# Optimization experiments

Hardware: AMD Instinct MI355X
Metric: run time of the kernel (lower is better)

The kernel has to match this reference:

```python
import jax, jax.numpy as jnp
import numpy as np

B, L, D = 2, 2048, 1024
H, DH = 16, 64
SCALE = 1.0 / np.sqrt(DH).astype(np.float32)
NEG = -1e9


def setup_inputs() -> dict:
    key = jax.random.key(0)
    ks = jax.random.split(key, 12)
    s = 0.02
    x = jax.random.normal(ks[0], (B, L, D), jnp.float32)
    lattice = jax.random.normal(ks[1], (B, 6), jnp.float32)
    B_graph = jax.random.normal(ks[2], (B, L, L), jnp.float32) * 0.05
    # causal additive mask [L, L]
    attn_mask = jnp.where(jnp.tril(jnp.ones((L, L), bool)), 0.0, NEG).astype(jnp.float32)
    Wq = jax.random.normal(ks[3], (D, H * DH), jnp.float32) * s
    bq = jnp.zeros((H * DH,), jnp.float32)
    Wk = jax.random.normal(ks[4], (D, H * DH), jnp.float32) * s
    bk = jnp.zeros((H * DH,), jnp.float32)
    Wv = jax.random.normal(ks[5], (D, H * DH), jnp.float32) * s
    bv = jnp.zeros((H * DH,), jnp.float32)
    Wo = jax.random.normal(ks[6], (H * DH, D), jnp.float32) * s
    bo = jnp.zeros((D,), jnp.float32)
    Wl = jax.random.normal(ks[7], (6, H), jnp.float32) * s
    bl = jnp.zeros((H,), jnp.float32)
    return {"x": x, "lattice": lattice, "B_graph": B_graph, "attn_mask": attn_mask,
            "Wq": Wq, "bq": bq, "Wk": Wk, "bk": bk, "Wv": Wv, "bv": bv,
            "Wo": Wo, "bo": bo, "Wl": Wl, "bl": bl}


def reference(x, lattice, B_graph, attn_mask, Wq, bq, Wk, bk, Wv, bv, Wo, bo, Wl, bl):
    b, l, d = x.shape
    # projections -> [b, h, l, dh]
    q = (x @ Wq + bq).reshape(b, l, H, DH).transpose(0, 2, 1, 3)
    k = (x @ Wk + bk).reshape(b, l, H, DH).transpose(0, 2, 1, 3)
    v = (x @ Wv + bv).reshape(b, l, H, DH).transpose(0, 2, 1, 3)
    scores = jnp.einsum('bhid,bhjd->bhij', q, k) * SCALE
    lattice_bias = lattice @ Wl + bl          # [b, h]
    scores = scores + lattice_bias[:, :, None, None]
    scores = scores + B_graph[:, None, :, :]   # [b,1,l,l]
    scores = scores + attn_mask[None, None, :, :]
    attn = jax.nn.softmax(scores.astype(jnp.float32), axis=-1).astype(scores.dtype)
    out = jnp.einsum('bhij,bhjd->bhid', attn, v)
    out = out.transpose(0, 2, 1, 3).reshape(b, l, H * DH)
    out = out @ Wo + bo
    return (out, attn)
```

## Files before the change

### kernel.cpp

```cpp
#include <hip/hip_runtime.h>
#include <stdint.h>
#include <stddef.h>

#define BB 2
#define LL 2048
#define DD 1024
#define HH 16
#define DHH 64
#define NH 1024

typedef __attribute__((ext_vector_type(8))) __bf16 bf16x8;
typedef __attribute__((ext_vector_type(4))) float f32x4;

__device__ __forceinline__ f32x4 mfma_bf16(bf16x8 a, bf16x8 b, f32x4 c) {
    return __builtin_amdgcn_mfma_f32_16x16x32_bf16(a, b, c, 0, 0, 0);
}

__device__ __forceinline__ unsigned short f2bf(float f) {
    union { float f; unsigned u; } v; v.f = f;
    unsigned r = v.u + 0x7FFFu + ((v.u >> 16) & 1u);
    return (unsigned short)(r >> 16);
}

__device__ __forceinline__ float bf2f(unsigned short s) {
    union { unsigned u; float f; } v; v.u = ((unsigned)s) << 16;
    return v.f;
}

__device__ __forceinline__ bf16x8 ld_frag(const unsigned short* p) {
    return *reinterpret_cast<const bf16x8*>(p);
}

__global__ __launch_bounds__(256)
void conv_x_kernel(const float* __restrict__ x, unsigned short* __restrict__ xb)
{
    const size_t i = ((size_t)blockIdx.x * 256 + threadIdx.x) * 8;
    float4 a = *(const float4*)(x + i);
    float4 b = *(const float4*)(x + i + 4);
    unsigned short t[8];
    t[0] = f2bf(a.x); t[1] = f2bf(a.y); t[2] = f2bf(a.z); t[3] = f2bf(a.w);
    t[4] = f2bf(b.x); t[5] = f2bf(b.y); t[6] = f2bf(b.z); t[7] = f2bf(b.w);
    *(int4*)(xb + i) = *(const int4*)t;
}

__global__ __launch_bounds__(256)
void conv_w_kernel(const float* __restrict__ W0, const float* __restrict__ W1,
                   const float* __restrict__ W2, const float* __restrict__ W3,
                   unsigned short* __restrict__ Wqkvt,
                   unsigned short* __restrict__ Wot)
{
    __shared__ unsigned short Ls[64][72];
    const int which = blockIdx.z;
    const float* W = (which == 0) ? W0 : (which == 1) ? W1 : (which == 2) ? W2 : W3;
    unsigned short* Wt = (which == 3) ? Wot : (Wqkvt + (size_t)which * 1024 * 1024);

    const int kt = blockIdx.x * 64, nt = blockIdx.y * 64;
    const int tid = threadIdx.x;

    {
        const int r = tid >> 2, c = (tid & 3) * 16;
        const float* wp = W + (size_t)(kt + r) * 1024 + nt + c;
        unsigned short t[16];
#pragma unroll
        for (int q = 0; q < 4; ++q) {
            float4 f = *(const float4*)(wp + q * 4);
            t[q * 4 + 0] = f2bf(f.x); t[q * 4 + 1] = f2bf(f.y);
            t[q * 4 + 2] = f2bf(f.z); t[q * 4 + 3] = f2bf(f.w);
        }
        *(int4*)&Ls[r][c]     = *(const int4*)&t[0];
        *(int4*)&Ls[r][c + 8] = *(const int4*)&t[8];
    }
    __syncthreads();
    {
        const int nr = tid >> 2, kc = (tid & 3) * 16;
        unsigned short t[16];
#pragma unroll
        for (int m = 0; m < 16; ++m) t[m] = Ls[kc + m][nr];
        unsigned short* op = Wt + (size_t)(nt + nr) * 1024 + kt + kc;
        *(int4*)op       = *(const int4*)&t[0];
        *(int4*)(op + 8) = *(const int4*)&t[8];
    }
}

template<int MODE>
__global__ __launch_bounds__(256)
void gemm128_kernel(const unsigned short* __restrict__ A,
                    const unsigned short* __restrict__ Bt,
                    const float* __restrict__ b0, const float* __restrict__ b1,
                    const float* __restrict__ b2,
                    void* __restrict__ outp)
{
    __shared__ __align__(16) unsigned short As[128][64];
    __shared__ __align__(16) unsigned short Bs[128][64];

    const int tid  = threadIdx.x;
    const int lane = tid & 63;
    const int w    = tid >> 6;
    const int wr   = w >> 1, wc = w & 1;
    const int l16  = lane & 15, lk = lane >> 4;

    const int m0 = blockIdx.y * 128;
    const int n0 = blockIdx.x * 128;

    const int r8  = tid >> 3;
    const int cb  = tid & 7;
    const int swz = cb ^ (r8 & 7);

    const unsigned short* Ap = A  + (size_t)m0 * 1024 + cb * 8;
    const unsigned short* Bp = Bt + (size_t)n0 * 1024 + cb * 8;

    f32x4 acc[4][4];
#pragma unroll
    for (int i = 0; i < 4; ++i)
#pragma unroll
        for (int j = 0; j < 4; ++j) acc[i][j] = f32x4{0.f, 0.f, 0.f, 0.f};

    for (int k0 = 0; k0 < 1024; k0 += 64) {
        __syncthreads();
#pragma unroll
        for (int c = 0; c < 4; ++c) {
            const int row = c * 32 + r8;
            bf16x8 av = ld_frag(Ap + (size_t)row * 1024 + k0);
            bf16x8 bv = ld_frag(Bp + (size_t)row * 1024 + k0);
            *(bf16x8*)&As[row][swz * 8] = av;
            *(bf16x8*)&Bs[row][swz * 8] = bv;
        }
        __syncthreads();

#pragma unroll
        for (int kk = 0; kk < 2; ++kk) {
            bf16x8 af[4], bfr[4];
#pragma unroll
            for (int fm = 0; fm < 4; ++fm) {
                const int row = wr * 64 + fm * 16 + l16;
                const int kb  = kk * 4 + lk;
                af[fm] = ld_frag(&As[row][(kb ^ (row & 7)) * 8]);
            }
#pragma unroll
            for (int fn = 0; fn < 4; ++fn) {
                const int row = wc * 64 + fn * 16 + l16;
                const int kb  = kk * 4 + lk;
                bfr[fn] = ld_frag(&Bs[row][(kb ^ (row & 7)) * 8]);
            }
#pragma unroll
            for (int fm = 0; fm < 4; ++fm)
#pragma unroll
                for (int fn = 0; fn < 4; ++fn)
                    acc[fm][fn] = mfma_bf16(af[fm], bfr[fn], acc[fm][fn]);
        }
    }

    if (MODE == 0) {
        const int which = n0 >> 10;
        const float* bias = (which == 0) ? b0 : (which == 1) ? b1 : b2;
        unsigned short* out = (unsigned short*)outp
                            + (size_t)which * ((size_t)BB * HH * LL * DHH);
        const int c00 = n0 & 1023;
#pragma unroll
        for (int fm = 0; fm < 4; ++fm)
#pragma unroll
            for (int fn = 0; fn < 4; ++fn)
#pragma unroll
                for (int r = 0; r < 4; ++r) {
                    const int grow = m0 + wr * 64 + fm * 16 + lk * 4 + r;
                    const int c    = c00 + wc * 64 + fn * 16 + l16;
                    const float v  = acc[fm][fn][r] + bias[c];
                    const int b = grow >> 11, i = grow & 2047;
                    const int h = c >> 6,     d = c & 63;
                    out[(((size_t)(b * HH + h)) * LL + i) * DHH + d] = f2bf(v);
                }
    } else {
        float* out = (float*)outp;
#pragma unroll
        for (int fm = 0; fm < 4; ++fm)
#pragma unroll
            for (int fn = 0; fn < 4; ++fn)
#pragma unroll
                for (int r = 0; r < 4; ++r) {
                    const int grow = m0 + wr * 64 + fm * 16 + lk * 4 + r;
                    const int gcol = n0 + wc * 64 + fn * 16 + l16;
                    out[(size_t)grow * DD + gcol] = acc[fm][fn][r] + b0[gcol];
                }
    }
}

__global__ __launch_bounds__(256)
void v_transpose_kernel(const unsigned short* __restrict__ vws,
                        unsigned short* __restrict__ vT)
{
    __shared__ unsigned short Ls[64][72];
    const int bh = blockIdx.y;
    const int i0 = blockIdx.x * 64;
    const int tid = threadIdx.x;

    {
        const int r = tid >> 2, c = (tid & 3) * 16;
        const unsigned short* vp = vws + ((size_t)bh * LL + i0 + r) * DHH + c;
        *(int4*)&Ls[r][c]     = *(const int4*)vp;
        *(int4*)&Ls[r][c + 8] = *(const int4*)(vp + 8);
    }
    __syncthreads();
    {
        const int d = tid >> 2, c = (tid & 3) * 16;
        unsigned short tmp[16];
#pragma unroll
        for (int m = 0; m < 16; ++m) tmp[m] = Ls[c + m][d];
        unsigned short* op = vT + ((size_t)bh * DHH + d) * LL + i0 + c;
        *(int4*)op       = *(const int4*)&tmp[0];
        *(int4*)(op + 8) = *(const int4*)&tmp[8];
    }
}

__global__ __launch_bounds__(128, 4)
void attn_kernel(const unsigned short* __restrict__ qws,
                 const unsigned short* __restrict__ kws,
                 const unsigned short* __restrict__ vT,
                 const float* __restrict__ B_graph,
                 const float* __restrict__ lattice,
                 const float* __restrict__ Wl,
                 const float* __restrict__ bl,
                 float* __restrict__ attn_out,
                 unsigned short* __restrict__ out_pre)
{
    const int n  = blockIdx.x;
    const int bh = n & 31;
    const int tb = n >> 5;
    const int kg = tb >> 3, tt = tb & 7;
    const int ib = 8 * kg + ((kg & 1) ? 7 - tt : tt);
    const int b = bh >> 4, h = bh & 15;
    const int i0 = ib * 32;
    const int nj = (ib >> 1) + 1;

    __shared__ unsigned short Ps[2][16][72];

    const int tid  = threadIdx.x;
    const int lane = tid & 63;
    const int w    = tid >> 6;
    const int l16  = lane & 15, lk = lane >> 4;

    float lb = bl[h];
#pragma unroll
    for (int t = 0; t < 6; ++t) lb += lattice[b * 6 + t] * Wl[t * HH + h];

    const int bhh = b * HH + h;
    const unsigned short* qbase = qws + ((size_t)bhh * LL + i0) * DHH;
    const unsigned short* kbase = kws + (size_t)bhh * LL * DHH;
    const unsigned short* vtb   = vT + (size_t)bhh * DHH * LL;
    const float* gb = B_graph + (size_t)b * LL * LL;

    bf16x8 qa0 = ld_frag(qbase + (size_t)(w * 16 + l16) * DHH + lk * 8);
    bf16x8 qa1 = ld_frag(qbase + (size_t)(w * 16 + l16) * DHH + 32 + lk * 8);

    const int gi0 = i0 + w * 16 + lk * 4;

    float s_run[4];
#pragma unroll
    for (int r = 0; r < 4; ++r) s_run[r] = 0.f;

    auto loadK = [&](int jb, bf16x8* kb) {
        const unsigned short* kt = kbase + (size_t)jb * 64 * DHH;
#pragma unroll
        for (int fn = 0; fn < 4; ++fn) {
            kb[2 * fn]     = ld_frag(kt + (size_t)(fn * 16 + l16) * DHH + lk * 8);
            kb[2 * fn + 1] = ld_frag(kt + (size_t)(fn * 16 + l16) * DHH + 32 + lk * 8);
        }
    };

    auto accumTile = [&](int jb, const bf16x8* kb) {
#pragma unroll
        for (int fn = 0; fn < 4; ++fn) {
            f32x4 z = {0.f, 0.f, 0.f, 0.f};
            z = mfma_bf16(qa0, kb[2 * fn], z);
            z = mfma_bf16(qa1, kb[2 * fn + 1], z);
            const int gj = jb * 64 + fn * 16 + l16;
#pragma unroll
            for (int r = 0; r < 4; ++r) {
                const int gi = gi0 + r;
                const float sv = fmaf(z[r], 0.125f, lb + gb[(size_t)gi * LL + gj]);
                s_run[r] += (gj > gi) ? 0.f : __expf(sv);
            }
        }
    };

    {
        int jb = 0;
        for (; jb + 2 <= nj; jb += 2) {
            bf16x8 k0[8], k1[8];
            loadK(jb, k0);
            loadK(jb + 1, k1);
            accumTile(jb, k0);
            accumTile(jb + 1, k1);
        }
        if (jb < nj) {
            bf16x8 k0[8];
            loadK(jb, k0);
            accumTile(jb, k0);
        }
    }
#pragma unroll
    for (int off = 1; off < 16; off <<= 1)
#pragma unroll
        for (int r = 0; r < 4; ++r) s_run[r] += __shfl_xor(s_run[r], off, 64);

    float inv_s[4];
#pragma unroll
    for (int r = 0; r < 4; ++r) inv_s[r] = 1.0f / s_run[r];

    f32x4 oacc[4];
#pragma unroll
    for (int fn = 0; fn < 4; ++fn) oacc[fn] = f32x4{0.f, 0.f, 0.f, 0.f};

    for (int jb = 0; jb < nj; ++jb) {
        bf16x8 kb[8];
        loadK(jb, kb);

#pragma unroll
        for (int fn = 0; fn < 4; ++fn) {
            f32x4 z = {0.f, 0.f, 0.f, 0.f};
            z = mfma_bf16(qa0, kb[2 * fn], z);
            z = mfma_bf16(qa1, kb[2 * fn + 1], z);
            const int gj = jb * 64 + fn * 16 + l16;
#pragma unroll
            for (int r = 0; r < 4; ++r) {
                const int gi = gi0 + r;
                const float sv = fmaf(z[r], 0.125f, lb + gb[(size_t)gi * LL + gj]);
                const float p = ((gj > gi) ? 0.f : __expf(sv)) * inv_s[r];
                Ps[w][lk * 4 + r][fn * 16 + l16] = f2bf(p);
            }
        }

        const int jc0 = jb * 64 + l16 * 4;
#pragma unroll
        for (int s = 0; s < 4; ++s) {
            const int row = s * 4 + lk;
            const int gi  = i0 + w * 16 + row;
            const unsigned short* pp = &Ps[w][row][l16 * 4];
            ushort4 pb = *(const ushort4*)pp;
            f32x4 pv;
            pv.x = bf2f(pb.x); pv.y = bf2f(pb.y);
            pv.z = bf2f(pb.z); pv.w = bf2f(pb.w);
            __builtin_nontemporal_store(
                pv, (f32x4*)&attn_out[((size_t)bhh * LL + gi) * LL + jc0]);
        }

        bf16x8 pa0 = ld_frag(&Ps[w][l16][lk * 8]);
        bf16x8 pa1 = ld_frag(&Ps[w][l16][32 + lk * 8]);
#pragma unroll
        for (int fn = 0; fn < 4; ++fn) {
            const unsigned short* vp = vtb + (size_t)(fn * 16 + l16) * LL + jb * 64;
            bf16x8 vb0 = ld_frag(vp + lk * 8);
            bf16x8 vb1 = ld_frag(vp + 32 + lk * 8);
            oacc[fn] = mfma_bf16(pa0, vb0, oacc[fn]);
            oacc[fn] = mfma_bf16(pa1, vb1, oacc[fn]);
        }
    }

    const int zc0 = nj * 64;
    if (zc0 < LL) {
        const int nz4 = (LL - zc0) >> 2;
        const f32x4 z4 = {0.f, 0.f, 0.f, 0.f};
        for (int row = 0; row < 32; ++row) {
            f32x4* zp = (f32x4*)(attn_out + ((size_t)bhh * LL + i0 + row) * LL + zc0);
            for (int c4 = tid; c4 < nz4; c4 += 128)
                __builtin_nontemporal_store(z4, &zp[c4]);
        }
    }

#pragma unroll
    for (int fn = 0; fn < 4; ++fn)
#pragma unroll
        for (int r = 0; r < 4; ++r) {
            const int gi = gi0 + r;
            const int d  = fn * 16 + l16;
            out_pre[((size_t)(b * LL + gi)) * NH + h * DHH + d] = f2bf(oacc[fn][r]);
        }
}

extern "C" void kernel_launch(void* const* d_in, const int* in_sizes, int n_in,
                              void* d_out, int out_size, void* d_ws, size_t ws_size,
                              hipStream_t stream)
{
    const float* x       = (const float*)d_in[0];
    const float* lattice = (const float*)d_in[1];
    const float* B_graph = (const float*)d_in[2];
    const float* Wq = (const float*)d_in[4];
    const float* bq = (const float*)d_in[5];
    const float* Wk = (const float*)d_in[6];
    const float* bk = (const float*)d_in[7];
    const float* Wv = (const float*)d_in[8];
    const float* bv = (const float*)d_in[9];
    const float* Wo = (const float*)d_in[10];
    const float* bo = (const float*)d_in[11];
    const float* Wl = (const float*)d_in[12];
    const float* bl = (const float*)d_in[13];

    float* out  = (float*)d_out;
    float* attn = out + (size_t)BB * LL * DD;

    const size_t PHL = (size_t)BB * HH * LL * DHH;
    unsigned short* qkv    = (unsigned short*)d_ws;
    unsigned short* qw     = qkv;
    unsigned short* kw     = qkv + PHL;
    unsigned short* vw     = qkv + 2 * PHL;
    unsigned short* outpre = qkv + 3 * PHL;
    unsigned short* Wqkvt  = outpre;
    unsigned short* xb     = outpre + (size_t)BB * LL * NH;
    unsigned short* vT     = xb;
    unsigned short* Wot    = xb + (size_t)BB * LL * DD;

    conv_x_kernel<<<dim3((BB * LL * DD) / (256 * 8)), 256, 0, stream>>>(x, xb);
    conv_w_kernel<<<dim3(16, 16, 4), 256, 0, stream>>>(Wq, Wk, Wv, Wo, Wqkvt, Wot);

    gemm128_kernel<0><<<dim3(3 * NH / 128, (BB * LL) / 128), 256, 0, stream>>>(
        xb, Wqkvt, bq, bk, bv, qkv);

    v_transpose_kernel<<<dim3(LL / 64, BB * HH), 256, 0, stream>>>(vw, vT);

    attn_kernel<<<dim3(BB * HH * (LL / 32)), 128, 0, stream>>>(
        qw, kw, vT, B_graph, lattice, Wl, bl, attn, outpre);

    gemm128_kernel<1><<<dim3(DD / 128, (BB * LL) / 128), 256, 0, stream>>>(
        outpre, Wot, bo, bo, bo, out);
}
```

Measured before the change: 330.4 us.

## Split attention key range across two wave pairs per block with LDS reduction

Doubles the attention block to 256 threads. Each pair of waves handles half of the causal key blocks for the same 32 query rows. Row sums and partial PV outputs are then combined through shared memory. This is meant to raise parallelism and latency hiding for the long serial key loop, especially for late query tiles. In exchange it adds two block barriers and LDS traffic, drops the previous two-tile K prefetch, and splits work unevenly when nj is odd.

```diff
diff --git a/kernel.cpp b/kernel.cpp
--- a/kernel.cpp
+++ b/kernel.cpp
@@ -211,7 +211,7 @@
     }
 }
 
-__global__ __launch_bounds__(128, 4)
+__global__ __launch_bounds__(256, 8)
 void attn_kernel(const unsigned short* __restrict__ qws,
                  const unsigned short* __restrict__ kws,
                  const unsigned short* __restrict__ vT,
@@ -231,12 +231,20 @@
     const int i0 = ib * 32;
     const int nj = (ib >> 1) + 1;
 
-    __shared__ unsigned short Ps[2][16][72];
+    __shared__ unsigned short Ps[4][16][72];
+    __shared__ float Sp[2][32];
+    __shared__ float Osum[2][16][68];
 
     const int tid  = threadIdx.x;
     const int lane = tid & 63;
     const int w    = tid >> 6;
+    const int rg   = w & 1;
+    const int jh   = w >> 1;
     const int l16  = lane & 15, lk = lane >> 4;
+
+    const int mid = (nj + 1) >> 1;
+    const int j0 = jh ? mid : 0;
+    const int j1 = jh ? nj : mid;
 
     float lb = bl[h];
 #pragma unroll
@@ -248,30 +256,24 @@
     const unsigned short* vtb   = vT + (size_t)bhh * DHH * LL;
     const float* gb = B_graph + (size_t)b * LL * LL;
 
-    bf16x8 qa0 = ld_frag(qbase + (size_t)(w * 16 + l16) * DHH + lk * 8);
-    bf16x8 qa1 = ld_frag(qbase + (size_t)(w * 16 + l16) * DHH + 32 + lk * 8);
-
-    const int gi0 = i0 + w * 16 + lk * 4;
+    bf16x8 qa0 = ld_frag(qbase + (size_t)(rg * 16 + l16) * DHH + lk * 8);
+    bf16x8 qa1 = ld_frag(qbase + (size_t)(rg * 16 + l16) * DHH + 32 + lk * 8);
+
+    const int gi0 = i0 + rg * 16 + lk * 4;
 
     float s_run[4];
 #pragma unroll
     for (int r = 0; r < 4; ++r) s_run[r] = 0.f;
 
-    auto loadK = [&](int jb, bf16x8* kb) {
+    for (int jb = j0; jb < j1; ++jb) {
         const unsigned short* kt = kbase + (size_t)jb * 64 * DHH;
 #pragma unroll
         for (int fn = 0; fn < 4; ++fn) {
-            kb[2 * fn]     = ld_frag(kt + (size_t)(fn * 16 + l16) * DHH + lk * 8);
-            kb[2 * fn + 1] = ld_frag(kt + (size_t)(fn * 16 + l16) * DHH + 32 + lk * 8);
-        }
-    };
-
-    auto accumTile = [&](int jb, const bf16x8* kb) {
-#pragma unroll
-        for (int fn = 0; fn < 4; ++fn) {
+            bf16x8 kb0 = ld_frag(kt + (size_t)(fn * 16 + l16) * DHH + lk * 8);
+            bf16x8 kb1 = ld_frag(kt + (size_t)(fn * 16 + l16) * DHH + 32 + lk * 8);
             f32x4 z = {0.f, 0.f, 0.f, 0.f};
-            z = mfma_bf16(qa0, kb[2 * fn], z);
-            z = mfma_bf16(qa1, kb[2 * fn + 1], z);
+            z = mfma_bf16(qa0, kb0, z);
+            z = mfma_bf16(qa1, kb1, z);
             const int gj = jb * 64 + fn * 16 + l16;
 #pragma unroll
             for (int r = 0; r < 4; ++r) {
@@ -280,45 +282,38 @@
                 s_run[r] += (gj > gi) ? 0.f : __expf(sv);
             }
         }
-    };
-
-    {
-        int jb = 0;
-        for (; jb + 2 <= nj; jb += 2) {
-            bf16x8 k0[8], k1[8];
-            loadK(jb, k0);
-            loadK(jb + 1, k1);
-            accumTile(jb, k0);
-            accumTile(jb + 1, k1);
-        }
-        if (jb < nj) {
-            bf16x8 k0[8];
-            loadK(jb, k0);
-            accumTile(jb, k0);
-        }
     }
 #pragma unroll
     for (int off = 1; off < 16; off <<= 1)
 #pragma unroll
         for (int r = 0; r < 4; ++r) s_run[r] += __shfl_xor(s_run[r], off, 64);
 
+    if (l16 == 0) {
+#pragma unroll
+        for (int r = 0; r < 4; ++r) Sp[jh][rg * 16 + lk * 4 + r] = s_run[r];
+    }
+    __syncthreads();
+
     float inv_s[4];
 #pragma unroll
-    for (int r = 0; r < 4; ++r) inv_s[r] = 1.0f / s_run[r];
+    for (int r = 0; r < 4; ++r) {
+        const int row = rg * 16 + lk * 4 + r;
+        inv_s[r] = 1.0f / (Sp[0][row] + Sp[1][row]);
+    }
 
     f32x4 oacc[4];
 #pragma unroll
     for (int fn = 0; fn < 4; ++fn) oacc[fn] = f32x4{0.f, 0.f, 0.f, 0.f};
 
-    for (int jb = 0; jb < nj; ++jb) {
-        bf16x8 kb[8];
-        loadK(jb, kb);
-
+    for (int jb = j0; jb < j1; ++jb) {
+        const unsigned short* kt = kbase + (size_t)jb * 64 * DHH;
 #pragma unroll
         for (int fn = 0; fn < 4; ++fn) {
+            bf16x8 kb0 = ld_frag(kt + (size_t)(fn * 16 + l16) * DHH + lk * 8);
+            bf16x8 kb1 = ld_frag(kt + (size_t)(fn * 16 + l16) * DHH + 32 + lk * 8);
             f32x4 z = {0.f, 0.f, 0.f, 0.f};
-            z = mfma_bf16(qa0, kb[2 * fn], z);
-            z = mfma_bf16(qa1, kb[2 * fn + 1], z);
+            z = mfma_bf16(qa0, kb0, z);
+            z = mfma_bf16(qa1, kb1, z);
             const int gj = jb * 64 + fn * 16 + l16;
 #pragma unroll
             for (int r = 0; r < 4; ++r) {
@@ -333,7 +328,7 @@
 #pragma unroll
         for (int s = 0; s < 4; ++s) {
             const int row = s * 4 + lk;
-            const int gi  = i0 + w * 16 + row;
+            const int gi  = i0 + rg * 16 + row;
             const unsigned short* pp = &Ps[w][row][l16 * 4];
             ushort4 pb = *(const ushort4*)pp;
             f32x4 pv;
@@ -355,25 +350,37 @@
         }
     }
 
+    if (jh == 1) {
+#pragma unroll
+        for (int fn = 0; fn < 4; ++fn)
+#pragma unroll
+            for (int r = 0; r < 4; ++r)
+                Osum[rg][lk * 4 + r][fn * 16 + l16] = oacc[fn][r];
+    }
+    __syncthreads();
+
     const int zc0 = nj * 64;
     if (zc0 < LL) {
         const int nz4 = (LL - zc0) >> 2;
         const f32x4 z4 = {0.f, 0.f, 0.f, 0.f};
         for (int row = 0; row < 32; ++row) {
             f32x4* zp = (f32x4*)(attn_out + ((size_t)bhh * LL + i0 + row) * LL + zc0);
-            for (int c4 = tid; c4 < nz4; c4 += 128)
+            for (int c4 = tid; c4 < nz4; c4 += 256)
                 __builtin_nontemporal_store(z4, &zp[c4]);
         }
     }
 
-#pragma unroll
-    for (int fn = 0; fn < 4; ++fn)
-#pragma unroll
-        for (int r = 0; r < 4; ++r) {
-            const int gi = gi0 + r;
-            const int d  = fn * 16 + l16;
-            out_pre[((size_t)(b * LL + gi)) * NH + h * DHH + d] = f2bf(oacc[fn][r]);
-        }
+    if (jh == 0) {
+#pragma unroll
+        for (int fn = 0; fn < 4; ++fn)
+#pragma unroll
+            for (int r = 0; r < 4; ++r) {
+                const float v = oacc[fn][r] + Osum[rg][lk * 4 + r][fn * 16 + l16];
+                const int gi = gi0 + r;
+                const int d  = fn * 16 + l16;
+                out_pre[((size_t)(b * LL + gi)) * NH + h * DHH + d] = f2bf(v);
+            }
+    }
 }
 
 extern "C" void kernel_launch(void* const* d_in, const int* in_sizes, int n_in,
@@ -416,7 +423,7 @@
 
     v_transpose_kernel<<<dim3(LL / 64, BB * HH), 256, 0, stream>>>(vw, vT);
 
-    attn_kernel<<<dim3(BB * HH * (LL / 32)), 128, 0, stream>>>(
+    attn_kernel<<<dim3(BB * HH * (LL / 32)), 256, 0, stream>>>(
         qw, kw, vT, B_graph, lattice, Wl, bl, attn, outpre);
 
     gemm128_kernel<1><<<dim3(DD / 128, (BB * LL) / 128), 256, 0, stream>>>(
```

After: 385.8 us. +16.8%, slower.
